# Performance work log

Measured on AMD Instinct MI355X. Metric: run time of the kernel, lower is better.

## Reference

```python
import jax, jax.numpy as jnp
import numpy as np


def setup_inputs() -> dict:
    key = jax.random.key(0)
    ks = jax.random.split(key, 4)
    B, S, D, H, E = 4, 2048, 1024, 4096, 4
    sd = 1.0 / np.sqrt(D)
    sh = 1.0 / np.sqrt(H)
    return {
        "x": jax.random.normal(ks[0], (B, S, D), jnp.float32),
        "Wr": jax.random.normal(ks[1], (D, E), jnp.float32) * sd,
        "W1": jax.random.normal(ks[2], (E, D, H), jnp.float32) * sd,
        "b1": jnp.zeros((E, H), jnp.float32),
        "W2": jax.random.normal(ks[3], (E, H, D), jnp.float32) * sh,
        "b2": jnp.zeros((E, D), jnp.float32),
        "top_k": 2,
    }


def reference(x, Wr, W1, b1, W2, b2, top_k):
    # Router: softmax over experts, then top-k + renormalize (as in torch code)
    logits = jnp.einsum("bsd,de->bse", x, Wr)              # [B,S,E]
    probs = jax.nn.softmax(logits, axis=-1)
    wk, idx = jax.lax.top_k(probs, top_k)                  # [B,S,K]
    wk = wk / jnp.sum(wk, axis=-1, keepdims=True)
    # Scatter top-k weights back to dense per-expert weights [B,S,E]
    E = probs.shape[-1]
    onehot = jax.nn.one_hot(idx, E, dtype=x.dtype)         # [B,S,K,E]
    weights = jnp.einsum("bsk,bske->bse", wk, onehot)      # [B,S,E]
    # Expert MLPs (Linear-ReLU-Linear), computed dense over experts and
    # combined with the (mostly-zero) routing weights — same math as the
    # gather/scatter loop in the torch module.
    h = jax.nn.relu(jnp.einsum("bsd,edh->bseh", x, W1) + b1)   # [B,S,E,H]
    y = jnp.einsum("bseh,ehd->bsed", h, W2) + b2               # [B,S,E,D]
    out = jnp.einsum("bse,bsed->bsd", weights, y)              # [B,S,D]
    aux_loss = jnp.asarray(0.0, dtype=x.dtype)
    return out, aux_loss
```

## Files before the change

kernel.cpp:

```cpp
#include <hip/hip_runtime.h>
#include <cstdint>
#include <cstddef>

typedef _Float16 f16;
typedef __attribute__((ext_vector_type(8))) f16 f16x8;
typedef __attribute__((ext_vector_type(4))) f16 f16x4;
typedef __attribute__((ext_vector_type(4))) float f32x4;

#define M_TOK 8192
#define DDIM 1024
#define HDIM 4096
#define NEXP 4
#define TOTPAD 17408

__device__ __forceinline__ void async_copy16(const void* g, void* s) {
    __builtin_amdgcn_global_load_lds((__attribute__((address_space(1))) void*)g,
                                     (__attribute__((address_space(3))) void*)s,
                                     16, 0, 0);
}

__device__ __forceinline__ f16x8 ds_read_b128_f16(uint32_t addr) {
    f16x8 r;
    asm volatile("ds_read_b128 %0, %1" : "=v"(r) : "v"(addr));
    return r;
}
__device__ __forceinline__ uint32_t lds_addr(const void* p) {
    return (uint32_t)(uintptr_t)(__attribute__((address_space(3))) const void*)p;
}

__device__ __forceinline__ void stage2(const f16* g0, const f16* g1, int koff,
                                       f16* plane, int tid) {
    async_copy16(g0 + koff, plane + tid * 8);
    async_copy16(g1 + koff, plane + 2048 + tid * 8);
}

__global__ __launch_bounds__(256) void router_kernel(
    const float* __restrict__ x, const float* __restrict__ Wr,
    float* __restrict__ wts, int* __restrict__ top2, float2* __restrict__ wpair) {
    __shared__ float wr_s[DDIM * NEXP];
    for (int i = threadIdx.x; i < DDIM * NEXP; i += 256) wr_s[i] = Wr[i];
    __syncthreads();
    const int wave = threadIdx.x >> 6, lane = threadIdx.x & 63;
    const int t = blockIdx.x * 4 + wave;
    float a0 = 0.f, a1 = 0.f, a2 = 0.f, a3 = 0.f;
    const float* xr = x + (size_t)t * DDIM;
    for (int i = 0; i < DDIM; i += 256) {
        const int d = i + lane * 4;
        const float4 v = *(const float4*)(xr + d);
        const float* w0 = &wr_s[d * 4];
        a0 += v.x * w0[0] + v.y * w0[4] + v.z * w0[8]  + v.w * w0[12];
        a1 += v.x * w0[1] + v.y * w0[5] + v.z * w0[9]  + v.w * w0[13];
        a2 += v.x * w0[2] + v.y * w0[6] + v.z * w0[10] + v.w * w0[14];
        a3 += v.x * w0[3] + v.y * w0[7] + v.z * w0[11] + v.w * w0[15];
    }
    for (int off = 32; off > 0; off >>= 1) {
        a0 += __shfl_xor(a0, off, 64);
        a1 += __shfl_xor(a1, off, 64);
        a2 += __shfl_xor(a2, off, 64);
        a3 += __shfl_xor(a3, off, 64);
    }
    if (lane == 0) {
        float lg[4] = {a0, a1, a2, a3};
        int i1 = 0;
        for (int e = 1; e < 4; ++e) if (lg[e] > lg[i1]) i1 = e;
        int i2 = -1;
        for (int e = 0; e < 4; ++e) {
            if (e == i1) continue;
            if (i2 < 0 || lg[e] > lg[i2]) i2 = e;
        }
        const float w1 = 1.0f / (1.0f + expf(lg[i2] - lg[i1]));
        float w[4] = {0.f, 0.f, 0.f, 0.f};
        w[i1] = w1; w[i2] = 1.0f - w1;
        float* o = wts + (size_t)t * 4;
        o[0] = w[0]; o[1] = w[1]; o[2] = w[2]; o[3] = w[3];
        top2[t] = i1 | (i2 << 8);
        wpair[t] = make_float2(w1, 1.0f - w1);
    }
}

__global__ __launch_bounds__(256) void count_kernel(
    const int* __restrict__ top2, int* __restrict__ meta) {
    __shared__ int lc[4];
    if (threadIdx.x < 4) lc[threadIdx.x] = 0;
    __syncthreads();
    const int t = blockIdx.x * 256 + threadIdx.x;
    const int p = top2[t];
    atomicAdd(&lc[p & 0xff], 1);
    atomicAdd(&lc[(p >> 8) & 0xff], 1);
    __syncthreads();
    if (threadIdx.x < 4) atomicAdd(&meta[threadIdx.x], lc[threadIdx.x]);
}

__global__ void offsets_kernel(int* __restrict__ meta) {
    if (threadIdx.x == 0) {
        int off = 0;
        for (int e = 0; e < 4; ++e) {
            const int c = meta[e];
            const int cp = (c + 127) & ~127;
            meta[4 + e] = cp;
            meta[8 + e] = off;
            off += cp;
        }
    }
}

__global__ __launch_bounds__(256) void fill_kernel(
    const int* __restrict__ top2, int* __restrict__ meta,
    int* __restrict__ toklist, int2* __restrict__ slotmap) {
    __shared__ int lc[4], base[4];
    if (threadIdx.x < 4) lc[threadIdx.x] = 0;
    __syncthreads();
    const int t = blockIdx.x * 256 + threadIdx.x;
    const int p = top2[t];
    const int e1 = p & 0xff, e2 = (p >> 8) & 0xff;
    const int r1 = atomicAdd(&lc[e1], 1);
    const int r2 = atomicAdd(&lc[e2], 1);
    __syncthreads();
    if (threadIdx.x < 4) base[threadIdx.x] = atomicAdd(&meta[12 + threadIdx.x], lc[threadIdx.x]);
    __syncthreads();
    const int p1 = meta[8 + e1] + base[e1] + r1;
    const int p2 = meta[8 + e2] + base[e2] + r2;
    toklist[p1] = t;
    toklist[p2] = t;
    slotmap[t] = make_int2(p1, p2);
}

__global__ __launch_bounds__(256) void convert_f16_kernel(
    const float* __restrict__ in, f16* __restrict__ out, int n4) {
    const int i = blockIdx.x * 256 + threadIdx.x;
    if (i < n4) {
        const float4 v = ((const float4*)in)[i];
        f16x4 o = {(f16)v.x, (f16)v.y, (f16)v.z, (f16)v.w};
        ((f16x4*)out)[i] = o;
    }
}

__global__ __launch_bounds__(256) void pack_nk_kernel(
    const float* __restrict__ in0, f16* __restrict__ out0, int K, int N) {
    __shared__ float tile[64][65];
    const float* in = in0 + (size_t)blockIdx.z * K * N;
    f16* out = out0 + (size_t)blockIdx.z * K * N;
    const int n0 = blockIdx.x * 64, k0 = blockIdx.y * 64;
    const int tx = threadIdx.x & 63, ty = threadIdx.x >> 6;
#pragma unroll
    for (int i = 0; i < 64; i += 4)
        tile[ty + i][tx] = in[(size_t)(k0 + ty + i) * N + n0 + tx];
    __syncthreads();
#pragma unroll
    for (int c = 0; c < 2; ++c) {
        const int cc = c * 256 + threadIdx.x;
        const int nl = cc >> 3, kc = cc & 7;
        f16x8 v;
#pragma unroll
        for (int j = 0; j < 8; ++j) v[j] = (f16)tile[kc * 8 + j][nl];
        *(f16x8*)&out[(size_t)(n0 + nl) * K + k0 + kc * 8] = v;
    }
}

template <int MODE>
__global__ __launch_bounds__(256, 2) void gemm128_kernel(
    const f16* __restrict__ A, const f16* __restrict__ Bt, int N, int K,
    const float* __restrict__ bias, f16* __restrict__ outH, float* __restrict__ outF,
    const float* __restrict__ wts, const int* __restrict__ toklist,
    const int* __restrict__ meta, int e0) {
    __shared__ __align__(16) f16 S[2][16384];
    const int zz = blockIdx.z;
    const int e = e0 + zz;
    const int m0 = blockIdx.x * 128, n0 = blockIdx.y * 128;
    int cnt = M_TOK, cp = M_TOK, off = 0;
    if (meta) { cnt = meta[e]; cp = meta[4 + e]; off = meta[8 + e]; }
    if (m0 >= cp) return;

    const f16* Be = Bt + (size_t)zz * N * K;
    const float* be = bias + (size_t)zz * N;

    const int tid = threadIdx.x;
    const int wave = tid >> 6, lane = tid & 63;
    const int wm = wave >> 1, wn = wave & 1;
    const int quad = lane >> 4, l16 = lane & 15;
    const int NT = K >> 6;

    const int r0 = tid >> 2;
    const int gswz = ((tid & 3) ^ ((r0 >> 1) & 3)) * 8;
    const f16* ga[2]; const f16* gb[2];
#pragma unroll
    for (int q = 0; q < 2; ++q) {
        const int gm = m0 + q * 64 + r0;
        int arow;
        if (MODE == 0) arow = toklist ? toklist[off + gm] : gm;
        else arow = off + gm;
        ga[q] = A + (size_t)arow * K + gswz;
        gb[q] = Be + (size_t)(n0 + q * 64 + r0) * K + gswz;
    }

    const int chq = ((quad ^ ((l16 >> 1) & 3)) << 3);
    const uint32_t sb0 = lds_addr(&S[0][0]), sb1 = lds_addr(&S[1][0]);
    const uint32_t a_b = (uint32_t)(((wm * 64 + l16) * 32 + chq) * 2);
    const uint32_t b_b = (uint32_t)(16384 + ((wn * 64 + l16) * 32 + chq) * 2);

    f32x4 acc[4][4] = {};

    stage2(ga[0], ga[1], 0,  S[0] + 0,     tid);
    stage2(gb[0], gb[1], 0,  S[0] + 8192,  tid);
    stage2(ga[0], ga[1], 32, S[0] + 4096,  tid);
    stage2(gb[0], gb[1], 32, S[0] + 12288, tid);
    if (NT > 1) {
        stage2(ga[0], ga[1], 64, S[1] + 0,     tid);
        stage2(gb[0], gb[1], 64, S[1] + 8192,  tid);
        stage2(ga[0], ga[1], 96, S[1] + 4096,  tid);
        asm volatile("s_waitcnt vmcnt(6)" ::: "memory");
    } else {
        asm volatile("s_waitcnt vmcnt(0)" ::: "memory");
    }
    __builtin_amdgcn_s_barrier();

    int p = 0;
#pragma unroll 1
    for (int t = 0; t < NT; ++t) {
        const uint32_t sp = p ? sb1 : sb0;
        f16* SpW = S[p];
        f16* SoW = S[p ^ 1];
        f16x8 af[4], bf0, bf1;
#pragma unroll
        for (int i = 0; i < 4; ++i) af[i] = ds_read_b128_f16(sp + a_b + i * 1024);
        bf0 = ds_read_b128_f16(sp + b_b);
        bf1 = ds_read_b128_f16(sp + b_b + 1024);
        if (t + 1 < NT) stage2(gb[0], gb[1], ((t + 1) << 6) + 32, SoW + 12288, tid);
        __builtin_amdgcn_s_barrier();
        asm volatile("s_waitcnt lgkmcnt(0)" ::: "memory");
        __builtin_amdgcn_sched_barrier(0);
        __builtin_amdgcn_s_setprio(1);
#pragma unroll
        for (int i = 0; i < 4; ++i) {
            acc[i][0] = __builtin_amdgcn_mfma_f32_16x16x32_f16(af[i], bf0, acc[i][0], 0, 0, 0);
            acc[i][1] = __builtin_amdgcn_mfma_f32_16x16x32_f16(af[i], bf1, acc[i][1], 0, 0, 0);
        }
        __builtin_amdgcn_s_setprio(0);
        __builtin_amdgcn_s_barrier();
        bf0 = ds_read_b128_f16(sp + b_b + 2048);
        bf1 = ds_read_b128_f16(sp + b_b + 3072);
        if (t + 2 < NT) stage2(ga[0], ga[1], (t + 2) << 6, SpW, tid);
        __builtin_amdgcn_s_barrier();
        asm volatile("s_waitcnt lgkmcnt(0)" ::: "memory");
        __builtin_amdgcn_sched_barrier(0);
        __builtin_amdgcn_s_setprio(1);
#pragma unroll
        for (int i = 0; i < 4; ++i) {
            acc[i][2] = __builtin_amdgcn_mfma_f32_16x16x32_f16(af[i], bf0, acc[i][2], 0, 0, 0);
            acc[i][3] = __builtin_amdgcn_mfma_f32_16x16x32_f16(af[i], bf1, acc[i][3], 0, 0, 0);
        }
        __builtin_amdgcn_s_setprio(0);
        __builtin_amdgcn_s_barrier();
#pragma unroll
        for (int i = 0; i < 4; ++i)
            af[i] = ds_read_b128_f16(sp + a_b + 8192 + i * 1024);
        bf0 = ds_read_b128_f16(sp + b_b + 8192);
        bf1 = ds_read_b128_f16(sp + b_b + 8192 + 1024);
        if (t + 2 < NT) stage2(gb[0], gb[1], (t + 2) << 6, SpW + 8192, tid);
        __builtin_amdgcn_s_barrier();
        asm volatile("s_waitcnt lgkmcnt(0)" ::: "memory");
        __builtin_amdgcn_sched_barrier(0);
        __builtin_amdgcn_s_setprio(1);
#pragma unroll
        for (int i = 0; i < 4; ++i) {
            acc[i][0] = __builtin_amdgcn_mfma_f32_16x16x32_f16(af[i], bf0, acc[i][0], 0, 0, 0);
            acc[i][1] = __builtin_amdgcn_mfma_f32_16x16x32_f16(af[i], bf1, acc[i][1], 0, 0, 0);
        }
        __builtin_amdgcn_s_setprio(0);
        __builtin_amdgcn_s_barrier();
        bf0 = ds_read_b128_f16(sp + b_b + 8192 + 2048);
        bf1 = ds_read_b128_f16(sp + b_b + 8192 + 3072);
        if (t + 2 < NT) stage2(ga[0], ga[1], ((t + 2) << 6) + 32, SpW + 4096, tid);
        __builtin_amdgcn_s_barrier();
        asm volatile("s_waitcnt lgkmcnt(0)" ::: "memory");
        __builtin_amdgcn_sched_barrier(0);
        __builtin_amdgcn_s_setprio(1);
#pragma unroll
        for (int i = 0; i < 4; ++i) {
            acc[i][2] = __builtin_amdgcn_mfma_f32_16x16x32_f16(af[i], bf0, acc[i][2], 0, 0, 0);
            acc[i][3] = __builtin_amdgcn_mfma_f32_16x16x32_f16(af[i], bf1, acc[i][3], 0, 0, 0);
        }
        __builtin_amdgcn_s_setprio(0);
        if (t + 2 < NT) asm volatile("s_waitcnt vmcnt(6)" ::: "memory");
        else            asm volatile("s_waitcnt vmcnt(0)" ::: "memory");
        __builtin_amdgcn_s_barrier();
        p ^= 1;
    }

#pragma unroll
    for (int i = 0; i < 4; ++i) {
        const int mb = m0 + wm * 64 + i * 16 + quad * 4;
#pragma unroll
        for (int j = 0; j < 4; ++j) {
            const int n = n0 + wn * 64 + j * 16 + l16;
            const float bv = be[n];
#pragma unroll
            for (int r = 0; r < 4; ++r) {
                const int m = mb + r;
                float v = acc[i][j][r] + bv;
                if (MODE == 0) {
                    v = v > 0.0f ? v : 0.0f;
                    outH[(size_t)(off + m) * N + n] = (f16)v;
                } else {
                    if (outH) {
                        outH[(size_t)(off + m) * N + n] = (f16)v;
                    } else if (m < cnt) {
                        atomicAdd(&outF[(size_t)m * N + n], wts[m * 4 + e] * v);
                    }
                }
            }
        }
    }
}

__global__ __launch_bounds__(256) void combine_kernel(
    const f16* __restrict__ yseg, const int2* __restrict__ slotmap,
    const float2* __restrict__ wpair, float* __restrict__ out, int aux_idx) {
    const int t = blockIdx.x;
    const int2 p = slotmap[t];
    const float2 w = wpair[t];
    const int d = threadIdx.x * 4;
    const f16x4 a = *(const f16x4*)&yseg[(size_t)p.x * DDIM + d];
    const f16x4 b = *(const f16x4*)&yseg[(size_t)p.y * DDIM + d];
    float4 o;
// ... 16 lines not shown
    const float* W2 = (const float*)d_in[4];
    const float* b2 = (const float*)d_in[5];
    float* out = (float*)d_out;

    char* ws = (char*)d_ws;
    float*  wts   = (float*)ws;
    int*    meta  = (int*)(ws + (128 << 10));
    int*    top2  = (int*)(ws + (132 << 10));
    int*    tokl  = (int*)(ws + (164 << 10));
    float2* wpair = (float2*)(ws + (240 << 10));
    int2*   slotm = (int2*)(ws + (304 << 10));
    f16*    xb    = (f16*)(ws + (512 << 10));
    const size_t MBs = 1ull << 20;
    const size_t base = (512 << 10) + 16 * MBs;

    const size_t SPARSE_NEED = (512 << 10) + 80 * MBs + (size_t)TOTPAD * HDIM * sizeof(f16);
    const bool sparse = ws_size >= SPARSE_NEED;

    const int aux_idx = (out_size == M_TOK * DDIM + 1) ? (M_TOK * DDIM) : -1;

    f16 *w1t, *w2t, *h, *yseg;
    if (sparse) {
        w1t  = (f16*)(ws + base);
        w2t  = (f16*)(ws + base + 32 * MBs);
        h    = (f16*)(ws + base + 64 * MBs);
        yseg = (f16*)(ws + (512 << 10));
    } else {
        w1t = (f16*)(ws + base);
        w2t = (f16*)(ws + base + 8 * MBs);
        h   = (f16*)(ws + base + 16 * MBs);
        yseg = nullptr;
    }

    router_kernel<<<M_TOK / 4, 256, 0, stream>>>(x, Wr, wts, top2, wpair);
    convert_f16_kernel<<<(M_TOK * DDIM / 4) / 256, 256, 0, stream>>>(x, xb, M_TOK * DDIM / 4);

    if (sparse) {
        hipMemsetAsync(meta, 0, 16 * sizeof(int), stream);
        hipMemsetAsync(tokl, 0, (size_t)TOTPAD * sizeof(int), stream);
        count_kernel<<<M_TOK / 256, 256, 0, stream>>>(top2, meta);
        offsets_kernel<<<1, 64, 0, stream>>>(meta);
        fill_kernel<<<M_TOK / 256, 256, 0, stream>>>(top2, meta, tokl, slotm);
        pack_nk_kernel<<<dim3(HDIM / 64, DDIM / 64, NEXP), 256, 0, stream>>>(W1, w1t, DDIM, HDIM);
        pack_nk_kernel<<<dim3(DDIM / 64, HDIM / 64, NEXP), 256, 0, stream>>>(W2, w2t, HDIM, DDIM);
        const int GX = TOTPAD / 128;
        gemm128_kernel<0><<<dim3(GX, HDIM / 128, NEXP), 256, 0, stream>>>(
            xb, w1t, HDIM, DDIM, b1, h, nullptr, wts, tokl, meta, 0);
        gemm128_kernel<1><<<dim3(GX, DDIM / 128, NEXP), 256, 0, stream>>>(
            h, w2t, DDIM, HDIM, b2, yseg, nullptr, wts, nullptr, meta, 0);
        combine_kernel<<<M_TOK, 256, 0, stream>>>(yseg, slotm, wpair, out, aux_idx);
    } else {
        hipMemsetAsync(out, 0, (size_t)out_size * sizeof(float), stream);
        for (int e = 0; e < NEXP; ++e) {
            pack_nk_kernel<<<dim3(HDIM / 64, DDIM / 64, 1), 256, 0, stream>>>(
                W1 + (size_t)e * DDIM * HDIM, w1t, DDIM, HDIM);
            gemm128_kernel<0><<<dim3(M_TOK / 128, HDIM / 128, 1), 256, 0, stream>>>(
                xb, w1t, HDIM, DDIM, b1 + (size_t)e * HDIM, h, nullptr, wts, nullptr, nullptr, e);
            pack_nk_kernel<<<dim3(DDIM / 64, HDIM / 64, 1), 256, 0, stream>>>(
                W2 + (size_t)e * HDIM * DDIM, w2t, HDIM, DDIM);
            gemm128_kernel<1><<<dim3(M_TOK / 128, DDIM / 128, 1), 256, 0, stream>>>(
                h, w2t, DDIM, HDIM, b2 + (size_t)e * DDIM, nullptr, out, wts, nullptr, nullptr, e);
        }
    }
}
```

Baseline: 610.6 us.

## Shrink expert GEMM tiles to 64x128 with two waves and reduce padding

The expert GEMMs now use 64x128 tiles with 128 threads (two waves) and a K-step of 32, instead of 128x128 tiles with 256 threads. Per-expert padding drops from 128 to 64 rows. The goal is less wasted MFMA work on padded rows and higher occupancy. The f32-to-f16 conversion of x is fused into the router kernel, and the offsets kernel is folded into the fill kernel, which removes two launches. The cost is less operand reuse per tile, more global loads per unit of FLOPs, and more barriers per unit of work.

```diff
diff --git a/kernel.cpp b/kernel.cpp
--- a/kernel.cpp
+++ b/kernel.cpp
@@ -11,7 +11,7 @@
 #define DDIM 1024
 #define HDIM 4096
 #define NEXP 4
-#define TOTPAD 17408
+#define TOTPAD 16640
 
 __device__ __forceinline__ void async_copy16(const void* g, void* s) {
     __builtin_amdgcn_global_load_lds((__attribute__((address_space(1))) void*)g,
@@ -28,15 +28,10 @@
     return (uint32_t)(uintptr_t)(__attribute__((address_space(3))) const void*)p;
 }
 
-__device__ __forceinline__ void stage2(const f16* g0, const f16* g1, int koff,
-                                       f16* plane, int tid) {
-    async_copy16(g0 + koff, plane + tid * 8);
-    async_copy16(g1 + koff, plane + 2048 + tid * 8);
-}
-
 __global__ __launch_bounds__(256) void router_kernel(
     const float* __restrict__ x, const float* __restrict__ Wr,
-    float* __restrict__ wts, int* __restrict__ top2, float2* __restrict__ wpair) {
+    float* __restrict__ wts, int* __restrict__ top2, float2* __restrict__ wpair,
+    f16* __restrict__ xb) {
     __shared__ float wr_s[DDIM * NEXP];
     for (int i = threadIdx.x; i < DDIM * NEXP; i += 256) wr_s[i] = Wr[i];
     __syncthreads();
@@ -44,9 +39,12 @@
     const int t = blockIdx.x * 4 + wave;
     float a0 = 0.f, a1 = 0.f, a2 = 0.f, a3 = 0.f;
     const float* xr = x + (size_t)t * DDIM;
+    f16* xo = xb + (size_t)t * DDIM;
     for (int i = 0; i < DDIM; i += 256) {
         const int d = i + lane * 4;
         const float4 v = *(const float4*)(xr + d);
+        f16x4 o = {(f16)v.x, (f16)v.y, (f16)v.z, (f16)v.w};
+        *(f16x4*)(xo + d) = o;
         const float* w0 = &wr_s[d * 4];
         a0 += v.x * w0[0] + v.y * w0[4] + v.z * w0[8]  + v.w * w0[12];
         a1 += v.x * w0[1] + v.y * w0[5] + v.z * w0[9]  + v.w * w0[13];
@@ -91,23 +89,10 @@
     if (threadIdx.x < 4) atomicAdd(&meta[threadIdx.x], lc[threadIdx.x]);
 }
 
-__global__ void offsets_kernel(int* __restrict__ meta) {
-    if (threadIdx.x == 0) {
-        int off = 0;
-        for (int e = 0; e < 4; ++e) {
-            const int c = meta[e];
-            const int cp = (c + 127) & ~127;
-            meta[4 + e] = cp;
-            meta[8 + e] = off;
-            off += cp;
-        }
-    }
-}
-
 __global__ __launch_bounds__(256) void fill_kernel(
     const int* __restrict__ top2, int* __restrict__ meta,
     int* __restrict__ toklist, int2* __restrict__ slotmap) {
-    __shared__ int lc[4], base[4];
+    __shared__ int lc[4], base[4], soff[4];
     if (threadIdx.x < 4) lc[threadIdx.x] = 0;
     __syncthreads();
     const int t = blockIdx.x * 256 + threadIdx.x;
@@ -116,23 +101,20 @@
     const int r1 = atomicAdd(&lc[e1], 1);
     const int r2 = atomicAdd(&lc[e2], 1);
     __syncthreads();
-    if (threadIdx.x < 4) base[threadIdx.x] = atomicAdd(&meta[12 + threadIdx.x], lc[threadIdx.x]);
-    __syncthreads();
-    const int p1 = meta[8 + e1] + base[e1] + r1;
-    const int p2 = meta[8 + e2] + base[e2] + r2;
+    if (threadIdx.x < 4) {
+        int offv = 0;
+        for (int q = 0; q < threadIdx.x; ++q) offv += (meta[q] + 63) & ~63;
+        soff[threadIdx.x] = offv;
+        base[threadIdx.x] = atomicAdd(&meta[12 + threadIdx.x], lc[threadIdx.x]);
+        meta[4 + threadIdx.x] = (meta[threadIdx.x] + 63) & ~63;
+        meta[8 + threadIdx.x] = offv;
+    }
+    __syncthreads();
+    const int p1 = soff[e1] + base[e1] + r1;
+    const int p2 = soff[e2] + base[e2] + r2;
     toklist[p1] = t;
     toklist[p2] = t;
     slotmap[t] = make_int2(p1, p2);
-}
-
-__global__ __launch_bounds__(256) void convert_f16_kernel(
-    const float* __restrict__ in, f16* __restrict__ out, int n4) {
-    const int i = blockIdx.x * 256 + threadIdx.x;
-    if (i < n4) {
-        const float4 v = ((const float4*)in)[i];
-        f16x4 o = {(f16)v.x, (f16)v.y, (f16)v.z, (f16)v.w};
-        ((f16x4*)out)[i] = o;
-    }
 }
 
 __global__ __launch_bounds__(256) void pack_nk_kernel(
@@ -158,15 +140,15 @@
 }
 
 template <int MODE>
-__global__ __launch_bounds__(256, 2) void gemm128_kernel(
+__global__ __launch_bounds__(128, 3) void gemm_kernel(
     const f16* __restrict__ A, const f16* __restrict__ Bt, int N, int K,
     const float* __restrict__ bias, f16* __restrict__ outH, float* __restrict__ outF,
     const float* __restrict__ wts, const int* __restrict__ toklist,
     const int* __restrict__ meta, int e0) {
-    __shared__ __align__(16) f16 S[2][16384];
+    __shared__ __align__(16) f16 S[2][8192];
     const int zz = blockIdx.z;
     const int e = e0 + zz;
-    const int m0 = blockIdx.x * 128, n0 = blockIdx.y * 128;
+    const int m0 = blockIdx.x * 64, n0 = blockIdx.y * 128;
     int cnt = M_TOK, cp = M_TOK, off = 0;
     if (meta) { cnt = meta[e]; cp = meta[4 + e]; off = meta[8 + e]; }
     if (m0 >= cp) return;
@@ -175,39 +157,45 @@
     const float* be = bias + (size_t)zz * N;
 
     const int tid = threadIdx.x;
-    const int wave = tid >> 6, lane = tid & 63;
-    const int wm = wave >> 1, wn = wave & 1;
+    const int wn = tid >> 6, lane = tid & 63;
     const int quad = lane >> 4, l16 = lane & 15;
-    const int NT = K >> 6;
+    const int NT = K >> 5;
 
     const int r0 = tid >> 2;
     const int gswz = ((tid & 3) ^ ((r0 >> 1) & 3)) * 8;
-    const f16* ga[2]; const f16* gb[2];
-#pragma unroll
-    for (int q = 0; q < 2; ++q) {
-        const int gm = m0 + q * 64 + r0;
+    const f16* ga[2]; const f16* gb[4];
+#pragma unroll
+    for (int g = 0; g < 2; ++g) {
+        const int gm = m0 + g * 32 + r0;
         int arow;
         if (MODE == 0) arow = toklist ? toklist[off + gm] : gm;
         else arow = off + gm;
-        ga[q] = A + (size_t)arow * K + gswz;
-        gb[q] = Be + (size_t)(n0 + q * 64 + r0) * K + gswz;
-    }
+        ga[g] = A + (size_t)arow * K + gswz;
+    }
+#pragma unroll
+    for (int g = 0; g < 4; ++g)
+        gb[g] = Be + (size_t)(n0 + g * 32 + r0) * K + gswz;
 
     const int chq = ((quad ^ ((l16 >> 1) & 3)) << 3);
     const uint32_t sb0 = lds_addr(&S[0][0]), sb1 = lds_addr(&S[1][0]);
-    const uint32_t a_b = (uint32_t)(((wm * 64 + l16) * 32 + chq) * 2);
-    const uint32_t b_b = (uint32_t)(16384 + ((wn * 64 + l16) * 32 + chq) * 2);
+    const uint32_t a_b = (uint32_t)((l16 * 32 + chq) * 2);
+    const uint32_t b_b = (uint32_t)((2048 + (wn * 64 + l16) * 32 + chq) * 2);
 
     f32x4 acc[4][4] = {};
 
-    stage2(ga[0], ga[1], 0,  S[0] + 0,     tid);
-    stage2(gb[0], gb[1], 0,  S[0] + 8192,  tid);
-    stage2(ga[0], ga[1], 32, S[0] + 4096,  tid);
-    stage2(gb[0], gb[1], 32, S[0] + 12288, tid);
+#define STAGE6(koff, buf)                                   \
+    do {                                                    \
+        async_copy16(ga[0] + (koff), (buf) + tid * 8);          \
+        async_copy16(ga[1] + (koff), (buf) + 1024 + tid * 8);   \
+        async_copy16(gb[0] + (koff), (buf) + 2048 + tid * 8);   \
+        async_copy16(gb[1] + (koff), (buf) + 3072 + tid * 8);   \
+        async_copy16(gb[2] + (koff), (buf) + 4096 + tid * 8);   \
+        async_copy16(gb[3] + (koff), (buf) + 5120 + tid * 8);   \
+    } while (0)
+
+    STAGE6(0, S[0]);
     if (NT > 1) {
-        stage2(ga[0], ga[1], 64, S[1] + 0,     tid);
-        stage2(gb[0], gb[1], 64, S[1] + 8192,  tid);
-        stage2(ga[0], ga[1], 96, S[1] + 4096,  tid);
+        STAGE6(32, S[1]);
         asm volatile("s_waitcnt vmcnt(6)" ::: "memory");
     } else {
         asm volatile("s_waitcnt vmcnt(0)" ::: "memory");
@@ -219,66 +207,28 @@
     for (int t = 0; t < NT; ++t) {
         const uint32_t sp = p ? sb1 : sb0;
         f16* SpW = S[p];
-        f16* SoW = S[p ^ 1];
-        f16x8 af[4], bf0, bf1;
+        f16x8 af[4], bf[4];
 #pragma unroll
         for (int i = 0; i < 4; ++i) af[i] = ds_read_b128_f16(sp + a_b + i * 1024);
-        bf0 = ds_read_b128_f16(sp + b_b);
-        bf1 = ds_read_b128_f16(sp + b_b + 1024);
-        if (t + 1 < NT) stage2(gb[0], gb[1], ((t + 1) << 6) + 32, SoW + 12288, tid);
+#pragma unroll
+        for (int j = 0; j < 4; ++j) bf[j] = ds_read_b128_f16(sp + b_b + j * 1024);
         __builtin_amdgcn_s_barrier();
         asm volatile("s_waitcnt lgkmcnt(0)" ::: "memory");
         __builtin_amdgcn_sched_barrier(0);
         __builtin_amdgcn_s_setprio(1);
 #pragma unroll
         for (int i = 0; i < 4; ++i) {
-            acc[i][0] = __builtin_amdgcn_mfma_f32_16x16x32_f16(af[i], bf0, acc[i][0], 0, 0, 0);
-            acc[i][1] = __builtin_amdgcn_mfma_f32_16x16x32_f16(af[i], bf1, acc[i][1], 0, 0, 0);
+            acc[i][0] = __builtin_amdgcn_mfma_f32_16x16x32_f16(af[i], bf[0], acc[i][0], 0, 0, 0);
+            acc[i][1] = __builtin_amdgcn_mfma_f32_16x16x32_f16(af[i], bf[1], acc[i][1], 0, 0, 0);
         }
         __builtin_amdgcn_s_setprio(0);
         __builtin_amdgcn_s_barrier();
-        bf0 = ds_read_b128_f16(sp + b_b + 2048);
-        bf1 = ds_read_b128_f16(sp + b_b + 3072);
-        if (t + 2 < NT) stage2(ga[0], ga[1], (t + 2) << 6, SpW, tid);
-        __builtin_amdgcn_s_barrier();
-        asm volatile("s_waitcnt lgkmcnt(0)" ::: "memory");
-        __builtin_amdgcn_sched_barrier(0);
+        if (t + 2 < NT) STAGE6((t + 2) << 5, SpW);
         __builtin_amdgcn_s_setprio(1);
 #pragma unroll
         for (int i = 0; i < 4; ++i) {
-            acc[i][2] = __builtin_amdgcn_mfma_f32_16x16x32_f16(af[i], bf0, acc[i][2], 0, 0, 0);
-            acc[i][3] = __builtin_amdgcn_mfma_f32_16x16x32_f16(af[i], bf1, acc[i][3], 0, 0, 0);
-        }
-        __builtin_amdgcn_s_setprio(0);
-        __builtin_amdgcn_s_barrier();
-#pragma unroll
-        for (int i = 0; i < 4; ++i)
-            af[i] = ds_read_b128_f16(sp + a_b + 8192 + i * 1024);
-        bf0 = ds_read_b128_f16(sp + b_b + 8192);
-        bf1 = ds_read_b128_f16(sp + b_b + 8192 + 1024);
-        if (t + 2 < NT) stage2(gb[0], gb[1], (t + 2) << 6, SpW + 8192, tid);
-        __builtin_amdgcn_s_barrier();
-        asm volatile("s_waitcnt lgkmcnt(0)" ::: "memory");
-        __builtin_amdgcn_sched_barrier(0);
-        __builtin_amdgcn_s_setprio(1);
-#pragma unroll
-        for (int i = 0; i < 4; ++i) {
-            acc[i][0] = __builtin_amdgcn_mfma_f32_16x16x32_f16(af[i], bf0, acc[i][0], 0, 0, 0);
-            acc[i][1] = __builtin_amdgcn_mfma_f32_16x16x32_f16(af[i], bf1, acc[i][1], 0, 0, 0);
-        }
-        __builtin_amdgcn_s_setprio(0);
-        __builtin_amdgcn_s_barrier();
-        bf0 = ds_read_b128_f16(sp + b_b + 8192 + 2048);
-        bf1 = ds_read_b128_f16(sp + b_b + 8192 + 3072);
-        if (t + 2 < NT) stage2(ga[0], ga[1], ((t + 2) << 6) + 32, SpW + 4096, tid);
-        __builtin_amdgcn_s_barrier();
-        asm volatile("s_waitcnt lgkmcnt(0)" ::: "memory");
-        __builtin_amdgcn_sched_barrier(0);
-        __builtin_amdgcn_s_setprio(1);
-#pragma unroll
-        for (int i = 0; i < 4; ++i) {
-            acc[i][2] = __builtin_amdgcn_mfma_f32_16x16x32_f16(af[i], bf0, acc[i][2], 0, 0, 0);
-            acc[i][3] = __builtin_amdgcn_mfma_f32_16x16x32_f16(af[i], bf1, acc[i][3], 0, 0, 0);
+            acc[i][2] = __builtin_amdgcn_mfma_f32_16x16x32_f16(af[i], bf[2], acc[i][2], 0, 0, 0);
+            acc[i][3] = __builtin_amdgcn_mfma_f32_16x16x32_f16(af[i], bf[3], acc[i][3], 0, 0, 0);
         }
         __builtin_amdgcn_s_setprio(0);
         if (t + 2 < NT) asm volatile("s_waitcnt vmcnt(6)" ::: "memory");
@@ -286,10 +236,11 @@
         __builtin_amdgcn_s_barrier();
         p ^= 1;
     }
+#undef STAGE6
 
 #pragma unroll
     for (int i = 0; i < 4; ++i) {
-        const int mb = m0 + wm * 64 + i * 16 + quad * 4;
+        const int mb = m0 + i * 16 + quad * 4;
 #pragma unroll
         for (int j = 0; j < 4; ++j) {
             const int n = n0 + wn * 64 + j * 16 + l16;
@@ -372,21 +323,19 @@
         yseg = nullptr;
     }
 
-    router_kernel<<<M_TOK / 4, 256, 0, stream>>>(x, Wr, wts, top2, wpair);
-    convert_f16_kernel<<<(M_TOK * DDIM / 4) / 256, 256, 0, stream>>>(x, xb, M_TOK * DDIM / 4);
+    router_kernel<<<M_TOK / 4, 256, 0, stream>>>(x, Wr, wts, top2, wpair, xb);
 
     if (sparse) {
         hipMemsetAsync(meta, 0, 16 * sizeof(int), stream);
         hipMemsetAsync(tokl, 0, (size_t)TOTPAD * sizeof(int), stream);
         count_kernel<<<M_TOK / 256, 256, 0, stream>>>(top2, meta);
-        offsets_kernel<<<1, 64, 0, stream>>>(meta);
         fill_kernel<<<M_TOK / 256, 256, 0, stream>>>(top2, meta, tokl, slotm);
         pack_nk_kernel<<<dim3(HDIM / 64, DDIM / 64, NEXP), 256, 0, stream>>>(W1, w1t, DDIM, HDIM);
         pack_nk_kernel<<<dim3(DDIM / 64, HDIM / 64, NEXP), 256, 0, stream>>>(W2, w2t, HDIM, DDIM);
-        const int GX = TOTPAD / 128;
-        gemm128_kernel<0><<<dim3(GX, HDIM / 128, NEXP), 256, 0, stream>>>(
+        const int GX = TOTPAD / 64;
+        gemm_kernel<0><<<dim3(GX, HDIM / 128, NEXP), 128, 0, stream>>>(
             xb, w1t, HDIM, DDIM, b1, h, nullptr, wts, tokl, meta, 0);
-        gemm128_kernel<1><<<dim3(GX, DDIM / 128, NEXP), 256, 0, stream>>>(
+        gemm_kernel<1><<<dim3(GX, DDIM / 128, NEXP), 128, 0, stream>>>(
             h, w2t, DDIM, HDIM, b2, yseg, nullptr, wts, nullptr, meta, 0);
         combine_kernel<<<M_TOK, 256, 0, stream>>>(yseg, slotm, wpair, out, aux_idx);
     } else {
@@ -394,11 +343,11 @@
         for (int e = 0; e < NEXP; ++e) {
             pack_nk_kernel<<<dim3(HDIM / 64, DDIM / 64, 1), 256, 0, stream>>>(
                 W1 + (size_t)e * DDIM * HDIM, w1t, DDIM, HDIM);
-            gemm128_kernel<0><<<dim3(M_TOK / 128, HDIM / 128, 1), 256, 0, stream>>>(
+            gemm_kernel<0><<<dim3(M_TOK / 64, HDIM / 128, 1), 128, 0, stream>>>(
                 xb, w1t, HDIM, DDIM, b1 + (size_t)e * HDIM, h, nullptr, wts, nullptr, nullptr, e);
             pack_nk_kernel<<<dim3(DDIM / 64, HDIM / 64, 1), 256, 0, stream>>>(
                 W2 + (size_t)e * HDIM * DDIM, w2t, HDIM, DDIM);
-            gemm128_kernel<1><<<dim3(M_TOK / 128, DDIM / 128, 1), 256, 0, stream>>>(
+            gemm_kernel<1><<<dim3(M_TOK / 64, DDIM / 128, 1), 128, 0, stream>>>(
                 h, w2t, DDIM, HDIM, b2 + (size_t)e * DDIM, nullptr, out, wts, nullptr, nullptr, e);
         }
     }
```

Result: slower. 752.3 us (+23.2%).

## Use 256x256 tile GEMM for first expert matmul and fuse small kernels

Applied to the files above, without the earlier changes.

Adds a 512-thread gemm256 kernel with 256x256 output tiles and a doubled LDS double buffer, used for the up-projection GEMM. Expert segments are now padded to 256 rows. The fp32-to-fp16 conversion of x moves into the router kernel, and the offsets kernel is folded into the fill kernel, which removes two launches and one full pass over x. The larger tile is meant to increase operand reuse per LDS load. It uses 128 KB of LDS per block, which may limit occupancy, and adds padding waste per expert.

```diff
diff --git a/kernel.cpp b/kernel.cpp
--- a/kernel.cpp
+++ b/kernel.cpp
@@ -28,15 +28,21 @@
     return (uint32_t)(uintptr_t)(__attribute__((address_space(3))) const void*)p;
 }
 
-__device__ __forceinline__ void stage2(const f16* g0, const f16* g1, int koff,
-                                       f16* plane, int tid) {
+__device__ __forceinline__ void stageP512(const f16* g0, const f16* g1, int koff,
+                                          f16* plane, int tid) {
+    async_copy16(g0 + koff, plane + tid * 8);
+    async_copy16(g1 + koff, plane + 4096 + tid * 8);
+}
+__device__ __forceinline__ void stageP256(const f16* g0, const f16* g1, int koff,
+                                          f16* plane, int tid) {
     async_copy16(g0 + koff, plane + tid * 8);
     async_copy16(g1 + koff, plane + 2048 + tid * 8);
 }
 
 __global__ __launch_bounds__(256) void router_kernel(
     const float* __restrict__ x, const float* __restrict__ Wr,
-    float* __restrict__ wts, int* __restrict__ top2, float2* __restrict__ wpair) {
+    float* __restrict__ wts, int* __restrict__ top2, float2* __restrict__ wpair,
+    f16* __restrict__ xb) {
     __shared__ float wr_s[DDIM * NEXP];
     for (int i = threadIdx.x; i < DDIM * NEXP; i += 256) wr_s[i] = Wr[i];
     __syncthreads();
@@ -44,9 +50,12 @@
     const int t = blockIdx.x * 4 + wave;
     float a0 = 0.f, a1 = 0.f, a2 = 0.f, a3 = 0.f;
     const float* xr = x + (size_t)t * DDIM;
+    f16* xo = xb + (size_t)t * DDIM;
     for (int i = 0; i < DDIM; i += 256) {
         const int d = i + lane * 4;
         const float4 v = *(const float4*)(xr + d);
+        f16x4 o = {(f16)v.x, (f16)v.y, (f16)v.z, (f16)v.w};
+        *(f16x4*)(xo + d) = o;
         const float* w0 = &wr_s[d * 4];
         a0 += v.x * w0[0] + v.y * w0[4] + v.z * w0[8]  + v.w * w0[12];
         a1 += v.x * w0[1] + v.y * w0[5] + v.z * w0[9]  + v.w * w0[13];
@@ -91,23 +100,10 @@
     if (threadIdx.x < 4) atomicAdd(&meta[threadIdx.x], lc[threadIdx.x]);
 }
 
-__global__ void offsets_kernel(int* __restrict__ meta) {
-    if (threadIdx.x == 0) {
-        int off = 0;
-        for (int e = 0; e < 4; ++e) {
-            const int c = meta[e];
-            const int cp = (c + 127) & ~127;
-            meta[4 + e] = cp;
-            meta[8 + e] = off;
-            off += cp;
-        }
-    }
-}
-
 __global__ __launch_bounds__(256) void fill_kernel(
     const int* __restrict__ top2, int* __restrict__ meta,
     int* __restrict__ toklist, int2* __restrict__ slotmap) {
-    __shared__ int lc[4], base[4];
+    __shared__ int lc[4], base[4], soff[4];
     if (threadIdx.x < 4) lc[threadIdx.x] = 0;
     __syncthreads();
     const int t = blockIdx.x * 256 + threadIdx.x;
@@ -116,23 +112,20 @@
     const int r1 = atomicAdd(&lc[e1], 1);
     const int r2 = atomicAdd(&lc[e2], 1);
     __syncthreads();
-    if (threadIdx.x < 4) base[threadIdx.x] = atomicAdd(&meta[12 + threadIdx.x], lc[threadIdx.x]);
-    __syncthreads();
-    const int p1 = meta[8 + e1] + base[e1] + r1;
-    const int p2 = meta[8 + e2] + base[e2] + r2;
+    if (threadIdx.x < 4) {
+        int offv = 0;
+        for (int q = 0; q < threadIdx.x; ++q) offv += (meta[q] + 255) & ~255;
+        soff[threadIdx.x] = offv;
+        base[threadIdx.x] = atomicAdd(&meta[12 + threadIdx.x], lc[threadIdx.x]);
+        meta[4 + threadIdx.x] = (meta[threadIdx.x] + 255) & ~255;
+        meta[8 + threadIdx.x] = offv;
+    }
+    __syncthreads();
+    const int p1 = soff[e1] + base[e1] + r1;
+    const int p2 = soff[e2] + base[e2] + r2;
     toklist[p1] = t;
     toklist[p2] = t;
     slotmap[t] = make_int2(p1, p2);
-}
-
-__global__ __launch_bounds__(256) void convert_f16_kernel(
-    const float* __restrict__ in, f16* __restrict__ out, int n4) {
-    const int i = blockIdx.x * 256 + threadIdx.x;
-    if (i < n4) {
-        const float4 v = ((const float4*)in)[i];
-        f16x4 o = {(f16)v.x, (f16)v.y, (f16)v.z, (f16)v.w};
-        ((f16x4*)out)[i] = o;
-    }
 }
 
 __global__ __launch_bounds__(256) void pack_nk_kernel(
@@ -154,6 +147,155 @@
 #pragma unroll
         for (int j = 0; j < 8; ++j) v[j] = (f16)tile[kc * 8 + j][nl];
         *(f16x8*)&out[(size_t)(n0 + nl) * K + k0 + kc * 8] = v;
+    }
+}
+
+template <int MODE>
+__global__ __launch_bounds__(512, 2) void gemm256_kernel(
+    const f16* __restrict__ A, const f16* __restrict__ Bt, int N, int K,
+    const float* __restrict__ bias, f16* __restrict__ outH, float* __restrict__ outF,
+    const float* __restrict__ wts, const int* __restrict__ toklist,
+    const int* __restrict__ meta, int e0) {
+    __shared__ __align__(16) f16 S[2][32768];
+    const int zz = blockIdx.z;
+    const int e = e0 + zz;
+    const int m0 = blockIdx.x * 256, n0 = blockIdx.y * 256;
+    int cnt = M_TOK, cp = M_TOK, off = 0;
+    if (meta) { cnt = meta[e]; cp = meta[4 + e]; off = meta[8 + e]; }
+    if (m0 >= cp) return;
+    (void)cnt;
+
+    const f16* Be = Bt + (size_t)zz * N * K;
+    const float* be = bias + (size_t)zz * N;
+
+    const int tid = threadIdx.x;
+    const int wave = tid >> 6, lane = tid & 63;
+    const int wm = wave >> 2, wn = wave & 3;
+    const int quad = lane >> 4, l16 = lane & 15;
+    const int NT = K >> 6;
+
+    const int r0 = tid >> 2;
+    const int gswz = ((tid & 3) ^ ((r0 >> 1) & 3)) * 8;
+    const f16* ga[2]; const f16* gb[2];
+#pragma unroll
+    for (int q = 0; q < 2; ++q) {
+        const int gm = m0 + q * 128 + r0;
+        int arow;
+        if (MODE == 0) arow = toklist ? toklist[off + gm] : gm;
+        else arow = off + gm;
+        ga[q] = A + (size_t)arow * K + gswz;
+        gb[q] = Be + (size_t)(n0 + q * 128 + r0) * K + gswz;
+    }
+
+    const int chq = ((quad ^ ((l16 >> 1) & 3)) << 3);
+    const uint32_t sb0 = lds_addr(&S[0][0]), sb1 = lds_addr(&S[1][0]);
+    const uint32_t a_b = (uint32_t)(((wm * 128 + l16) * 32 + chq) * 2);
+    const uint32_t b_b = (uint32_t)((16384 + (wn * 64 + l16) * 32 + chq) * 2);
+
+    f32x4 acc[8][4] = {};
+
+    stageP512(ga[0], ga[1], 0,  S[0] + 0,     tid);
+    stageP512(gb[0], gb[1], 0,  S[0] + 16384, tid);
+    stageP512(ga[0], ga[1], 32, S[0] + 8192,  tid);
+    stageP512(gb[0], gb[1], 32, S[0] + 24576, tid);
+    if (NT > 1) {
+        stageP512(ga[0], ga[1], 64, S[1] + 0,     tid);
+        stageP512(gb[0], gb[1], 64, S[1] + 16384, tid);
+        stageP512(ga[0], ga[1], 96, S[1] + 8192,  tid);
+        asm volatile("s_waitcnt vmcnt(6)" ::: "memory");
+    } else {
+        asm volatile("s_waitcnt vmcnt(0)" ::: "memory");
+    }
+    __builtin_amdgcn_s_barrier();
+
+    int p = 0;
+#pragma unroll 1
+    for (int t = 0; t < NT; ++t) {
+        const uint32_t sp = p ? sb1 : sb0;
+        f16* SpW = S[p];
+        f16* SoW = S[p ^ 1];
+        f16x8 af[8], bf0, bf1;
+#pragma unroll
+        for (int i = 0; i < 8; ++i) af[i] = ds_read_b128_f16(sp + a_b + i * 1024);
+        bf0 = ds_read_b128_f16(sp + b_b);
+        bf1 = ds_read_b128_f16(sp + b_b + 1024);
+        if (t + 1 < NT) stageP512(gb[0], gb[1], ((t + 1) << 6) + 32, SoW + 24576, tid);
+        __builtin_amdgcn_s_barrier();
+        asm volatile("s_waitcnt lgkmcnt(0)" ::: "memory");
+        __builtin_amdgcn_sched_barrier(0);
+        __builtin_amdgcn_s_setprio(1);
+#pragma unroll
+        for (int i = 0; i < 8; ++i) {
+            acc[i][0] = __builtin_amdgcn_mfma_f32_16x16x32_f16(af[i], bf0, acc[i][0], 0, 0, 0);
+            acc[i][1] = __builtin_amdgcn_mfma_f32_16x16x32_f16(af[i], bf1, acc[i][1], 0, 0, 0);
+        }
+        __builtin_amdgcn_s_setprio(0);
+        __builtin_amdgcn_s_barrier();
+        bf0 = ds_read_b128_f16(sp + b_b + 2048);
+        bf1 = ds_read_b128_f16(sp + b_b + 3072);
+        if (t + 2 < NT) stageP512(ga[0], ga[1], (t + 2) << 6, SpW, tid);
+        __builtin_amdgcn_s_barrier();
+        asm volatile("s_waitcnt lgkmcnt(0)" ::: "memory");
+        __builtin_amdgcn_sched_barrier(0);
+        __builtin_amdgcn_s_setprio(1);
+#pragma unroll
+        for (int i = 0; i < 8; ++i) {
+            acc[i][2] = __builtin_amdgcn_mfma_f32_16x16x32_f16(af[i], bf0, acc[i][2], 0, 0, 0);
+            acc[i][3] = __builtin_amdgcn_mfma_f32_16x16x32_f16(af[i], bf1, acc[i][3], 0, 0, 0);
+        }
+        __builtin_amdgcn_s_setprio(0);
+        __builtin_amdgcn_s_barrier();
+#pragma unroll
+        for (int i = 0; i < 8; ++i)
+            af[i] = ds_read_b128_f16(sp + a_b + 16384 + i * 1024);
+        bf0 = ds_read_b128_f16(sp + b_b + 16384);
+        bf1 = ds_read_b128_f16(sp + b_b + 16384 + 1024);
+        if (t + 2 < NT) stageP512(gb[0], gb[1], (t + 2) << 6, SpW + 16384, tid);
+        __builtin_amdgcn_s_barrier();
+        asm volatile("s_waitcnt lgkmcnt(0)" ::: "memory");
+        __builtin_amdgcn_sched_barrier(0);
+        __builtin_amdgcn_s_setprio(1);
+#pragma unroll
+        for (int i = 0; i < 8; ++i) {
+            acc[i][0] = __builtin_amdgcn_mfma_f32_16x16x32_f16(af[i], bf0, acc[i][0], 0, 0, 0);
+            acc[i][1] = __builtin_amdgcn_mfma_f32_16x16x32_f16(af[i], bf1, acc[i][1], 0, 0, 0);
+        }
+        __builtin_amdgcn_s_setprio(0);
+        __builtin_amdgcn_s_barrier();
+        bf0 = ds_read_b128_f16(sp + b_b + 16384 + 2048);
+        bf1 = ds_read_b128_f16(sp + b_b + 16384 + 3072);
+        if (t + 2 < NT) stageP512(ga[0], ga[1], ((t + 2) << 6) + 32, SpW + 8192, tid);
+        __builtin_amdgcn_s_barrier();
+        asm volatile("s_waitcnt lgkmcnt(0)" ::: "memory");
+        __builtin_amdgcn_sched_barrier(0);
+        __builtin_amdgcn_s_setprio(1);
+#pragma unroll
+        for (int i = 0; i < 8; ++i) {
+            acc[i][2] = __builtin_amdgcn_mfma_f32_16x16x32_f16(af[i], bf0, acc[i][2], 0, 0, 0);
+            acc[i][3] = __builtin_amdgcn_mfma_f32_16x16x32_f16(af[i], bf1, acc[i][3], 0, 0, 0);
+        }
+        __builtin_amdgcn_s_setprio(0);
+        if (t + 2 < NT) asm volatile("s_waitcnt vmcnt(6)" ::: "memory");
+        else            asm volatile("s_waitcnt vmcnt(0)" ::: "memory");
+        __builtin_amdgcn_s_barrier();
+        p ^= 1;
+    }
+
+#pragma unroll
+    for (int i = 0; i < 8; ++i) {
+        const int mb = m0 + wm * 128 + i * 16 + quad * 4;
+#pragma unroll
+        for (int j = 0; j < 4; ++j) {
+            const int n = n0 + wn * 64 + j * 16 + l16;
+            const float bv = be[n];
+#pragma unroll
+            for (int r = 0; r < 4; ++r) {
+                const int m = mb + r;
+                float v = acc[i][j][r] + bv;
+                v = v > 0.0f ? v : 0.0f;
+                outH[(size_t)(off + m) * N + n] = (f16)v;
+            }
+        }
     }
 }
 
@@ -196,18 +338,18 @@
     const int chq = ((quad ^ ((l16 >> 1) & 3)) << 3);
     const uint32_t sb0 = lds_addr(&S[0][0]), sb1 = lds_addr(&S[1][0]);
     const uint32_t a_b = (uint32_t)(((wm * 64 + l16) * 32 + chq) * 2);
-    const uint32_t b_b = (uint32_t)(16384 + ((wn * 64 + l16) * 32 + chq) * 2);
+    const uint32_t b_b = (uint32_t)((8192 + (wn * 64 + l16) * 32 + chq) * 2);
 
     f32x4 acc[4][4] = {};
 
-    stage2(ga[0], ga[1], 0,  S[0] + 0,     tid);
-    stage2(gb[0], gb[1], 0,  S[0] + 8192,  tid);
-    stage2(ga[0], ga[1], 32, S[0] + 4096,  tid);
-    stage2(gb[0], gb[1], 32, S[0] + 12288, tid);
+    stageP256(ga[0], ga[1], 0,  S[0] + 0,     tid);
+    stageP256(gb[0], gb[1], 0,  S[0] + 8192,  tid);
+    stageP256(ga[0], ga[1], 32, S[0] + 4096,  tid);
+    stageP256(gb[0], gb[1], 32, S[0] + 12288, tid);
     if (NT > 1) {
-        stage2(ga[0], ga[1], 64, S[1] + 0,     tid);
-        stage2(gb[0], gb[1], 64, S[1] + 8192,  tid);
-        stage2(ga[0], ga[1], 96, S[1] + 4096,  tid);
+        stageP256(ga[0], ga[1], 64, S[1] + 0,     tid);
+        stageP256(gb[0], gb[1], 64, S[1] + 8192,  tid);
+        stageP256(ga[0], ga[1], 96, S[1] + 4096,  tid);
         asm volatile("s_waitcnt vmcnt(6)" ::: "memory");
     } else {
         asm volatile("s_waitcnt vmcnt(0)" ::: "memory");
@@ -225,7 +367,7 @@
         for (int i = 0; i < 4; ++i) af[i] = ds_read_b128_f16(sp + a_b + i * 1024);
         bf0 = ds_read_b128_f16(sp + b_b);
         bf1 = ds_read_b128_f16(sp + b_b + 1024);
-        if (t + 1 < NT) stage2(gb[0], gb[1], ((t + 1) << 6) + 32, SoW + 12288, tid);
+        if (t + 1 < NT) stageP256(gb[0], gb[1], ((t + 1) << 6) + 32, SoW + 12288, tid);
         __builtin_amdgcn_s_barrier();
         asm volatile("s_waitcnt lgkmcnt(0)" ::: "memory");
         __builtin_amdgcn_sched_barrier(0);
@@ -239,7 +381,7 @@
         __builtin_amdgcn_s_barrier();
         bf0 = ds_read_b128_f16(sp + b_b + 2048);
         bf1 = ds_read_b128_f16(sp + b_b + 3072);
-        if (t + 2 < NT) stage2(ga[0], ga[1], (t + 2) << 6, SpW, tid);
+        if (t + 2 < NT) stageP256(ga[0], ga[1], (t + 2) << 6, SpW, tid);
         __builtin_amdgcn_s_barrier();
         asm volatile("s_waitcnt lgkmcnt(0)" ::: "memory");
         __builtin_amdgcn_sched_barrier(0);
@@ -256,7 +398,7 @@
             af[i] = ds_read_b128_f16(sp + a_b + 8192 + i * 1024);
         bf0 = ds_read_b128_f16(sp + b_b + 8192);
         bf1 = ds_read_b128_f16(sp + b_b + 8192 + 1024);
-        if (t + 2 < NT) stage2(gb[0], gb[1], (t + 2) << 6, SpW + 8192, tid);
+        if (t + 2 < NT) stageP256(gb[0], gb[1], (t + 2) << 6, SpW + 8192, tid);
         __builtin_amdgcn_s_barrier();
         asm volatile("s_waitcnt lgkmcnt(0)" ::: "memory");
         __builtin_amdgcn_sched_barrier(0);
@@ -270,7 +412,7 @@
         __builtin_amdgcn_s_barrier();
         bf0 = ds_read_b128_f16(sp + b_b + 8192 + 2048);
         bf1 = ds_read_b128_f16(sp + b_b + 8192 + 3072);
-        if (t + 2 < NT) stage2(ga[0], ga[1], ((t + 2) << 6) + 32, SpW + 4096, tid);
+        if (t + 2 < NT) stageP256(ga[0], ga[1], ((t + 2) << 6) + 32, SpW + 4096, tid);
         __builtin_amdgcn_s_barrier();
         asm volatile("s_waitcnt lgkmcnt(0)" ::: "memory");
         __builtin_amdgcn_sched_barrier(0);
@@ -372,21 +514,18 @@
         yseg = nullptr;
     }
 
-    router_kernel<<<M_TOK / 4, 256, 0, stream>>>(x, Wr, wts, top2, wpair);
-    convert_f16_kernel<<<(M_TOK * DDIM / 4) / 256, 256, 0, stream>>>(x, xb, M_TOK * DDIM / 4);
+    router_kernel<<<M_TOK / 4, 256, 0, stream>>>(x, Wr, wts, top2, wpair, xb);
 
     if (sparse) {
         hipMemsetAsync(meta, 0, 16 * sizeof(int), stream);
         hipMemsetAsync(tokl, 0, (size_t)TOTPAD * sizeof(int), stream);
         count_kernel<<<M_TOK / 256, 256, 0, stream>>>(top2, meta);
-        offsets_kernel<<<1, 64, 0, stream>>>(meta);
         fill_kernel<<<M_TOK / 256, 256, 0, stream>>>(top2, meta, tokl, slotm);
         pack_nk_kernel<<<dim3(HDIM / 64, DDIM / 64, NEXP), 256, 0, stream>>>(W1, w1t, DDIM, HDIM);
         pack_nk_kernel<<<dim3(DDIM / 64, HDIM / 64, NEXP), 256, 0, stream>>>(W2, w2t, HDIM, DDIM);
-        const int GX = TOTPAD / 128;
-        gemm128_kernel<0><<<dim3(GX, HDIM / 128, NEXP), 256, 0, stream>>>(
+        gemm256_kernel<0><<<dim3(TOTPAD / 256, HDIM / 256, NEXP), 512, 0, stream>>>(
             xb, w1t, HDIM, DDIM, b1, h, nullptr, wts, tokl, meta, 0);
-        gemm128_kernel<1><<<dim3(GX, DDIM / 128, NEXP), 256, 0, stream>>>(
+        gemm128_kernel<1><<<dim3(TOTPAD / 128, DDIM / 128, NEXP), 256, 0, stream>>>(
             h, w2t, DDIM, HDIM, b2, yseg, nullptr, wts, nullptr, meta, 0);
         combine_kernel<<<M_TOK, 256, 0, stream>>>(yseg, slotm, wpair, out, aux_idx);
     } else {
```

After: 607.1 us. No clear change (-0.6%).

## Fuse f16 conversion into router, fold offsets into fill, remap GEMM tiles per XCD

Applied to the files above, without the earlier changes.

The router kernel now writes the f16 copy of x while it reads x for the logits, so the separate conversion kernel and its second full pass over x are gone. The per-expert padded offsets are now computed inside fill_kernel, which removes the single-thread offsets kernel launch. The GEMM kernel also remaps its linear block index so that consecutive logical tiles land on the same XCD under round-robin dispatch, aiming for better L2 reuse of the A and B panels. The remap assumes the tile count divides by 8, and early-exit padding blocks are now spread across the grid instead of grouped together.

```diff
diff --git a/kernel.cpp b/kernel.cpp
--- a/kernel.cpp
+++ b/kernel.cpp
@@ -28,15 +28,16 @@
     return (uint32_t)(uintptr_t)(__attribute__((address_space(3))) const void*)p;
 }
 
-__device__ __forceinline__ void stage2(const f16* g0, const f16* g1, int koff,
-                                       f16* plane, int tid) {
+__device__ __forceinline__ void stageP256(const f16* g0, const f16* g1, int koff,
+                                          f16* plane, int tid) {
     async_copy16(g0 + koff, plane + tid * 8);
     async_copy16(g1 + koff, plane + 2048 + tid * 8);
 }
 
 __global__ __launch_bounds__(256) void router_kernel(
     const float* __restrict__ x, const float* __restrict__ Wr,
-    float* __restrict__ wts, int* __restrict__ top2, float2* __restrict__ wpair) {
+    float* __restrict__ wts, int* __restrict__ top2, float2* __restrict__ wpair,
+    f16* __restrict__ xb) {
     __shared__ float wr_s[DDIM * NEXP];
     for (int i = threadIdx.x; i < DDIM * NEXP; i += 256) wr_s[i] = Wr[i];
     __syncthreads();
@@ -44,9 +45,12 @@
     const int t = blockIdx.x * 4 + wave;
     float a0 = 0.f, a1 = 0.f, a2 = 0.f, a3 = 0.f;
     const float* xr = x + (size_t)t * DDIM;
+    f16* xo = xb + (size_t)t * DDIM;
     for (int i = 0; i < DDIM; i += 256) {
         const int d = i + lane * 4;
         const float4 v = *(const float4*)(xr + d);
+        f16x4 o = {(f16)v.x, (f16)v.y, (f16)v.z, (f16)v.w};
+        *(f16x4*)(xo + d) = o;
         const float* w0 = &wr_s[d * 4];
         a0 += v.x * w0[0] + v.y * w0[4] + v.z * w0[8]  + v.w * w0[12];
         a1 += v.x * w0[1] + v.y * w0[5] + v.z * w0[9]  + v.w * w0[13];
@@ -91,23 +95,10 @@
     if (threadIdx.x < 4) atomicAdd(&meta[threadIdx.x], lc[threadIdx.x]);
 }
 
-__global__ void offsets_kernel(int* __restrict__ meta) {
-    if (threadIdx.x == 0) {
-        int off = 0;
-        for (int e = 0; e < 4; ++e) {
-            const int c = meta[e];
-            const int cp = (c + 127) & ~127;
-            meta[4 + e] = cp;
-            meta[8 + e] = off;
-            off += cp;
-        }
-    }
-}
-
 __global__ __launch_bounds__(256) void fill_kernel(
     const int* __restrict__ top2, int* __restrict__ meta,
     int* __restrict__ toklist, int2* __restrict__ slotmap) {
-    __shared__ int lc[4], base[4];
+    __shared__ int lc[4], base[4], soff[4];
     if (threadIdx.x < 4) lc[threadIdx.x] = 0;
     __syncthreads();
     const int t = blockIdx.x * 256 + threadIdx.x;
@@ -116,23 +107,20 @@
     const int r1 = atomicAdd(&lc[e1], 1);
     const int r2 = atomicAdd(&lc[e2], 1);
     __syncthreads();
-    if (threadIdx.x < 4) base[threadIdx.x] = atomicAdd(&meta[12 + threadIdx.x], lc[threadIdx.x]);
-    __syncthreads();
-    const int p1 = meta[8 + e1] + base[e1] + r1;
-    const int p2 = meta[8 + e2] + base[e2] + r2;
+    if (threadIdx.x < 4) {
+        int offv = 0;
+        for (int q = 0; q < threadIdx.x; ++q) offv += (meta[q] + 127) & ~127;
+        soff[threadIdx.x] = offv;
+        base[threadIdx.x] = atomicAdd(&meta[12 + threadIdx.x], lc[threadIdx.x]);
+        meta[4 + threadIdx.x] = (meta[threadIdx.x] + 127) & ~127;
+        meta[8 + threadIdx.x] = offv;
+    }
+    __syncthreads();
+    const int p1 = soff[e1] + base[e1] + r1;
+    const int p2 = soff[e2] + base[e2] + r2;
     toklist[p1] = t;
     toklist[p2] = t;
     slotmap[t] = make_int2(p1, p2);
-}
-
-__global__ __launch_bounds__(256) void convert_f16_kernel(
-    const float* __restrict__ in, f16* __restrict__ out, int n4) {
-    const int i = blockIdx.x * 256 + threadIdx.x;
-    if (i < n4) {
-        const float4 v = ((const float4*)in)[i];
-        f16x4 o = {(f16)v.x, (f16)v.y, (f16)v.z, (f16)v.w};
-        ((f16x4*)out)[i] = o;
-    }
 }
 
 __global__ __launch_bounds__(256) void pack_nk_kernel(
@@ -166,7 +154,11 @@
     __shared__ __align__(16) f16 S[2][16384];
     const int zz = blockIdx.z;
     const int e = e0 + zz;
-    const int m0 = blockIdx.x * 128, n0 = blockIdx.y * 128;
+    const unsigned tot = gridDim.x * gridDim.y;
+    const unsigned f = blockIdx.x + blockIdx.y * gridDim.x;
+    const unsigned lg = (f & 7) * (tot >> 3) + (f >> 3);
+    const int m0 = (int)(lg % gridDim.x) * 128;
+    const int n0 = (int)(lg / gridDim.x) * 128;
     int cnt = M_TOK, cp = M_TOK, off = 0;
     if (meta) { cnt = meta[e]; cp = meta[4 + e]; off = meta[8 + e]; }
     if (m0 >= cp) return;
@@ -196,18 +188,18 @@
     const int chq = ((quad ^ ((l16 >> 1) & 3)) << 3);
     const uint32_t sb0 = lds_addr(&S[0][0]), sb1 = lds_addr(&S[1][0]);
     const uint32_t a_b = (uint32_t)(((wm * 64 + l16) * 32 + chq) * 2);
-    const uint32_t b_b = (uint32_t)(16384 + ((wn * 64 + l16) * 32 + chq) * 2);
+    const uint32_t b_b = (uint32_t)((8192 + (wn * 64 + l16) * 32 + chq) * 2);
 
     f32x4 acc[4][4] = {};
 
-    stage2(ga[0], ga[1], 0,  S[0] + 0,     tid);
-    stage2(gb[0], gb[1], 0,  S[0] + 8192,  tid);
-    stage2(ga[0], ga[1], 32, S[0] + 4096,  tid);
-    stage2(gb[0], gb[1], 32, S[0] + 12288, tid);
+    stageP256(ga[0], ga[1], 0,  S[0] + 0,     tid);
+    stageP256(gb[0], gb[1], 0,  S[0] + 8192,  tid);
+    stageP256(ga[0], ga[1], 32, S[0] + 4096,  tid);
+    stageP256(gb[0], gb[1], 32, S[0] + 12288, tid);
     if (NT > 1) {
-        stage2(ga[0], ga[1], 64, S[1] + 0,     tid);
-        stage2(gb[0], gb[1], 64, S[1] + 8192,  tid);
-        stage2(ga[0], ga[1], 96, S[1] + 4096,  tid);
+        stageP256(ga[0], ga[1], 64, S[1] + 0,     tid);
+        stageP256(gb[0], gb[1], 64, S[1] + 8192,  tid);
+        stageP256(ga[0], ga[1], 96, S[1] + 4096,  tid);
         asm volatile("s_waitcnt vmcnt(6)" ::: "memory");
     } else {
         asm volatile("s_waitcnt vmcnt(0)" ::: "memory");
@@ -225,7 +217,7 @@
         for (int i = 0; i < 4; ++i) af[i] = ds_read_b128_f16(sp + a_b + i * 1024);
         bf0 = ds_read_b128_f16(sp + b_b);
         bf1 = ds_read_b128_f16(sp + b_b + 1024);
-        if (t + 1 < NT) stage2(gb[0], gb[1], ((t + 1) << 6) + 32, SoW + 12288, tid);
+        if (t + 1 < NT) stageP256(gb[0], gb[1], ((t + 1) << 6) + 32, SoW + 12288, tid);
         __builtin_amdgcn_s_barrier();
         asm volatile("s_waitcnt lgkmcnt(0)" ::: "memory");
         __builtin_amdgcn_sched_barrier(0);
@@ -239,7 +231,7 @@
         __builtin_amdgcn_s_barrier();
         bf0 = ds_read_b128_f16(sp + b_b + 2048);
         bf1 = ds_read_b128_f16(sp + b_b + 3072);
-        if (t + 2 < NT) stage2(ga[0], ga[1], (t + 2) << 6, SpW, tid);
+        if (t + 2 < NT) stageP256(ga[0], ga[1], (t + 2) << 6, SpW, tid);
         __builtin_amdgcn_s_barrier();
         asm volatile("s_waitcnt lgkmcnt(0)" ::: "memory");
         __builtin_amdgcn_sched_barrier(0);
@@ -256,7 +248,7 @@
             af[i] = ds_read_b128_f16(sp + a_b + 8192 + i * 1024);
         bf0 = ds_read_b128_f16(sp + b_b + 8192);
         bf1 = ds_read_b128_f16(sp + b_b + 8192 + 1024);
-        if (t + 2 < NT) stage2(gb[0], gb[1], (t + 2) << 6, SpW + 8192, tid);
+        if (t + 2 < NT) stageP256(gb[0], gb[1], (t + 2) << 6, SpW + 8192, tid);
         __builtin_amdgcn_s_barrier();
         asm volatile("s_waitcnt lgkmcnt(0)" ::: "memory");
         __builtin_amdgcn_sched_barrier(0);
@@ -270,7 +262,7 @@
         __builtin_amdgcn_s_barrier();
         bf0 = ds_read_b128_f16(sp + b_b + 8192 + 2048);
         bf1 = ds_read_b128_f16(sp + b_b + 8192 + 3072);
-        if (t + 2 < NT) stage2(ga[0], ga[1], ((t + 2) << 6) + 32, SpW + 4096, tid);
+        if (t + 2 < NT) stageP256(ga[0], ga[1], ((t + 2) << 6) + 32, SpW + 4096, tid);
         __builtin_amdgcn_s_barrier();
         asm volatile("s_waitcnt lgkmcnt(0)" ::: "memory");
         __builtin_amdgcn_sched_barrier(0);
@@ -372,21 +364,18 @@
         yseg = nullptr;
     }
 
-    router_kernel<<<M_TOK / 4, 256, 0, stream>>>(x, Wr, wts, top2, wpair);
-    convert_f16_kernel<<<(M_TOK * DDIM / 4) / 256, 256, 0, stream>>>(x, xb, M_TOK * DDIM / 4);
+    router_kernel<<<M_TOK / 4, 256, 0, stream>>>(x, Wr, wts, top2, wpair, xb);
 
     if (sparse) {
         hipMemsetAsync(meta, 0, 16 * sizeof(int), stream);
         hipMemsetAsync(tokl, 0, (size_t)TOTPAD * sizeof(int), stream);
         count_kernel<<<M_TOK / 256, 256, 0, stream>>>(top2, meta);
-        offsets_kernel<<<1, 64, 0, stream>>>(meta);
         fill_kernel<<<M_TOK / 256, 256, 0, stream>>>(top2, meta, tokl, slotm);
         pack_nk_kernel<<<dim3(HDIM / 64, DDIM / 64, NEXP), 256, 0, stream>>>(W1, w1t, DDIM, HDIM);
         pack_nk_kernel<<<dim3(DDIM / 64, HDIM / 64, NEXP), 256, 0, stream>>>(W2, w2t, HDIM, DDIM);
-        const int GX = TOTPAD / 128;
-        gemm128_kernel<0><<<dim3(GX, HDIM / 128, NEXP), 256, 0, stream>>>(
+        gemm128_kernel<0><<<dim3(TOTPAD / 128, HDIM / 128, NEXP), 256, 0, stream>>>(
             xb, w1t, HDIM, DDIM, b1, h, nullptr, wts, tokl, meta, 0);
-        gemm128_kernel<1><<<dim3(GX, DDIM / 128, NEXP), 256, 0, stream>>>(
+        gemm128_kernel<1><<<dim3(TOTPAD / 128, DDIM / 128, NEXP), 256, 0, stream>>>(
             h, w2t, DDIM, HDIM, b2, yseg, nullptr, wts, nullptr, meta, 0);
         combine_kernel<<<M_TOK, 256, 0, stream>>>(yseg, slotm, wpair, out, aux_idx);
     } else {
```

After: 623.8 us. 2.2% more time.
